# Optimization experiments

Hardware: AMD Instinct MI355X
Metric: run time of the kernel (lower is better)

The kernel has to match this reference:

```python
import jax, jax.numpy as jnp
import numpy as np
from jax.scipy.linalg import solve_triangular

B, T, D = 4, 8192, 1024
HEAD_DIM = 128
CHUNK = 64


def setup_inputs() -> dict:
    key = jax.random.key(0)
    ks = jax.random.split(key, 8)
    H = D // HEAD_DIM
    x = jax.random.normal(ks[0], (B, T, D), dtype=jnp.float32)
    W_write = jax.random.normal(ks[1], (D, D), dtype=jnp.float32) * 0.02
    W_gate = jax.random.normal(ks[2], (H, D), dtype=jnp.float32) * 0.02
    W_out = jax.random.normal(ks[3], (D, D), dtype=jnp.float32) * 0.02
    W_beta = jax.random.normal(ks[4], (H, D), dtype=jnp.float32) * 0.02
    W_alpha = jax.random.normal(ks[5], (H, D), dtype=jnp.float32) * 0.02
    # dt_bias init as in torch: dt ~ loguniform(1e-3, 1e-1), bias = dt + log(-expm1(-dt))
    u = jax.random.uniform(ks[6], (H,), dtype=jnp.float32)
    dt = jnp.exp(u * (jnp.log(jnp.float32(0.1)) - jnp.log(jnp.float32(0.001))) + jnp.log(jnp.float32(0.001)))
    dt_bias = dt + jnp.log(-jnp.expm1(-dt))
    A_log = jnp.log(jax.random.uniform(ks[7], (H,), dtype=jnp.float32, minval=1e-3, maxval=16.0))
    return {"x": x, "W_write": W_write, "W_gate": W_gate, "W_out": W_out,
            "W_beta": W_beta, "W_alpha": W_alpha, "dt_bias": dt_bias, "A_log": A_log}


def reference(x, W_write, W_gate, W_out, W_beta, W_alpha, dt_bias, A_log):
    Bn, Tn, Dm = x.shape
    H = A_log.shape[0]
    d = Dm // H
    C = CHUNK
    assert Tn % C == 0
    N = Tn // C

    xf = x.astype(jnp.float32)
    v = (xf @ W_write.T).reshape(Bn, Tn, H, d)                       # write values
    gate = jax.nn.sigmoid(xf @ W_gate.T)[..., None]                  # (B,T,H,1)
    beta = jax.nn.sigmoid(xf @ W_beta.T)                             # (B,T,H)
    decay = -jnp.exp(A_log) * jax.nn.softplus(xf @ W_alpha.T + dt_bias)  # (B,T,H)

    rk = xf.reshape(Bn, Tn, H, d)
    rk = rk / jnp.maximum(jnp.linalg.norm(rk, axis=-1, keepdims=True), 1e-12)
    wk = jnp.pad(rk[:, :-1], ((0, 0), (1, 0), (0, 0), (0, 0)))       # token-shifted write key

    # (B,H,T,d)
    rk = rk.transpose(0, 2, 1, 3)
    wk = wk.transpose(0, 2, 1, 3)
    v = v.transpose(0, 2, 1, 3)
    bt = beta.transpose(0, 2, 1)[..., None]
    v = v * bt
    wk_beta = wk * bt

    # chunked: (B,H,N,C,d)
    rk = rk.reshape(Bn, H, N, C, d)
    wk = wk.reshape(Bn, H, N, C, d)
    v = v.reshape(Bn, H, N, C, d)
    wk_beta = wk_beta.reshape(Bn, H, N, C, d)
    dec = jnp.cumsum(decay.transpose(0, 2, 1).reshape(Bn, H, N, C), axis=-1)  # cumulative log-decay
    dec_exp = jnp.exp(dec)[..., None]

    lower = jnp.tril(jnp.ones((C, C), dtype=bool))            # incl. diagonal
    strict_lower = jnp.tril(jnp.ones((C, C), dtype=bool), -1)
    diff = dec[..., :, None] - dec[..., None, :]
    L_mask = jnp.exp(jnp.where(lower, diff, -jnp.inf))        # (B,H,N,C,C), 0 above diag

    # UT transform: torch's in-place row loop computes (I + M_strict)^{-1}
    M = jnp.einsum('bhnid,bhnjd->bhnij', wk_beta, wk) * L_mask
    M = jnp.where(strict_lower, M, jnp.float32(0.0))
    eye = jnp.eye(C, dtype=jnp.float32)
    A = solve_triangular(eye + M, jnp.broadcast_to(eye, M.shape), lower=True)

    v = A @ v
    wk_cumdecay = A @ (wk_beta * dec_exp)

    # sequential inter-chunk recurrence over N chunks, carrying matrix state S
    xs = (rk.transpose(2, 0, 1, 3, 4), wk.transpose(2, 0, 1, 3, 4), v.transpose(2, 0, 1, 3, 4),
          wk_cumdecay.transpose(2, 0, 1, 3, 4), dec.transpose(2, 0, 1, 3), L_mask.transpose(2, 0, 1, 3, 4))
    S0 = jnp.zeros((Bn, H, d, d), dtype=jnp.float32)

    def step(S, inp):
        rk_i, wk_i, v_i, wkcd_i, dec_i, L_i = inp
        attn = jnp.einsum('bhid,bhjd->bhij', rk_i, wk_i) * L_i
        attn = jnp.where(lower, attn, jnp.float32(0.0))
        v_new = v_i - wkcd_i @ S
        o_i = (rk_i * jnp.exp(dec_i)[..., None]) @ S + attn @ v_new
        dw = jnp.exp(dec_i[..., -1:] - dec_i)[..., None]                  # (B,H,C,1)
        S_new = S * jnp.exp(dec_i[..., -1])[..., None, None] + jnp.einsum('bhcd,bhce->bhde', wk_i * dw, v_new)
        return S_new, o_i

    _, o = jax.lax.scan(step, S0, xs)                 # (N,B,H,C,d)
    o = o.transpose(1, 2, 0, 3, 4).reshape(Bn, H, Tn, d).transpose(0, 2, 1, 3)  # (B,T,H,d)
    o = (o * gate).reshape(Bn, Tn, Dm)
    return (x + (o @ W_out.T)).astype(x.dtype)
```

## Files before the change

### kernel.cpp

```cpp
#include <hip/hip_runtime.h>
#include <math.h>

#define B_ 4
#define T_ 8192
#define D_ 1024
#define H_ 8
#define HD_ 128
#define C_ 64
#define N_ 128
#define BT_ (B_*T_)
#define BH_ (B_*H_)

typedef unsigned short ushort_t;
typedef unsigned long long ull_t;
typedef short s8v __attribute__((ext_vector_type(8)));
typedef float f32x4 __attribute__((ext_vector_type(4)));

__device__ __forceinline__ void fma4(float4& a, float s, const float4& v) {
  a.x += s*v.x; a.y += s*v.y; a.z += s*v.z; a.w += s*v.w;
}
__device__ __forceinline__ float bfu(unsigned int u16) {
  return __uint_as_float(u16 << 16);
}
__device__ __forceinline__ ushort_t f2bf(float f) {
  unsigned int x = __float_as_uint(f);
  x += 0x7FFFu + ((x >> 16) & 1u);
  return (ushort_t)(x >> 16);
}
__device__ __forceinline__ ull_t pack4bf(float a, float b, float c, float d) {
  return (ull_t)f2bf(a) | ((ull_t)f2bf(b) << 16) | ((ull_t)f2bf(c) << 32) | ((ull_t)f2bf(d) << 48);
}

__global__ __launch_bounds__(256) void k1_proj(
    const float* __restrict__ x, const float* __restrict__ Wg,
    const float* __restrict__ Wb, const float* __restrict__ Wa,
    const float* __restrict__ dt_bias, const float* __restrict__ A_log,
    float* __restrict__ gate_buf, float* __restrict__ beta_buf,
    float* __restrict__ decay_buf, float* __restrict__ innorm_buf) {
  const int row = blockIdx.x;
  const int b = row / T_, t = row % T_;
  const int tid = threadIdx.x;
  __shared__ float xs[D_];
  __shared__ float red[3][H_][4];
  __shared__ float scal[3][H_];
  __shared__ float rnorm[H_];

  ((float4*)xs)[tid] = ((const float4*)(x + (size_t)row * D_))[tid];
  __syncthreads();

  float pg[H_], pb[H_], pa[H_];
  #pragma unroll
  for (int h = 0; h < H_; h++) { pg[h] = 0.f; pb[h] = 0.f; pa[h] = 0.f; }
  for (int i = tid; i < D_; i += 256) {
    float xv = xs[i];
    #pragma unroll
    for (int h = 0; h < H_; h++) {
      pg[h] += xv * Wg[h*D_ + i];
      pb[h] += xv * Wb[h*D_ + i];
      pa[h] += xv * Wa[h*D_ + i];
    }
  }
  const int lane = tid & 63, wv = tid >> 6;
  #pragma unroll
  for (int h = 0; h < H_; h++) {
    float g = pg[h], bb = pb[h], aa = pa[h];
    #pragma unroll
    for (int off = 32; off > 0; off >>= 1) {
      g  += __shfl_down(g, off);
      bb += __shfl_down(bb, off);
      aa += __shfl_down(aa, off);
    }
    if (lane == 0) { red[0][h][wv] = g; red[1][h][wv] = bb; red[2][h][wv] = aa; }
  }
  float pn;
  {
    int hh = tid >> 5, e0 = (tid & 31) * 4;
    const float* xh = xs + hh*HD_ + e0;
    pn = xh[0]*xh[0] + xh[1]*xh[1] + xh[2]*xh[2] + xh[3]*xh[3];
  }
  #pragma unroll
  for (int off = 16; off > 0; off >>= 1) pn += __shfl_down(pn, off, 32);
  __syncthreads();
  if ((tid & 31) == 0) rnorm[tid >> 5] = fmaxf(sqrtf(pn), 1e-12f);
  if (tid < 24) {
    int p = tid >> 3, h = tid & 7;
    scal[p][h] = red[p][h][0] + red[p][h][1] + red[p][h][2] + red[p][h][3];
  }
  __syncthreads();
  if (tid < H_) {
    int h = tid;
    float g  = 1.f / (1.f + expf(-scal[0][h]));
    float be = 1.f / (1.f + expf(-scal[1][h]));
    float z  = scal[2][h] + dt_bias[h];
    float sp = (z > 20.f) ? z : log1pf(expf(z));
    float dc = -expf(A_log[h]) * sp;
    size_t idx = (size_t)(b*H_ + h)*T_ + t;
    gate_buf[idx] = g; beta_buf[idx] = be; decay_buf[idx] = dc;
    innorm_buf[idx] = 1.f / rnorm[h];
  }
}

__global__ __launch_bounds__(256) void k_gemm_bf16(
    const float* __restrict__ A, const float* __restrict__ W,
    const float* __restrict__ R, float* __restrict__ C,
    int M, int N, int K) {
  __shared__ ushort_t La[128*40];
  __shared__ ushort_t Lw[128*40];
  const int tid = threadIdx.x;
  const int w = tid >> 6, lane = tid & 63;
  const int l15 = lane & 15, l4 = lane >> 4;
  const int wr = w >> 1, wc = w & 1;

  const int nwg = gridDim.x;
  const int NB = N >> 7;
  const int bid = blockIdx.x;
  const int swz = (bid & 7) * (nwg >> 3) + (bid >> 3);
  const int row0 = (swz / NB) * 128, col0 = (swz % NB) * 128;

  f32x4 acc[4][4];
  #pragma unroll
  for (int m = 0; m < 4; m++)
    #pragma unroll
    for (int n = 0; n < 4; n++)
      #pragma unroll
      for (int r = 0; r < 4; r++) acc[m][n][r] = 0.f;

  float4 pa[2][2], pw[2][2];
  auto LOAD = [&](int k0) {
    #pragma unroll
    for (int s = 0; s < 2; s++) {
      int slot = tid + s*256;
      int rw = slot >> 2, kg = (slot & 3) * 8;
      const float* ap = A + (size_t)(row0 + rw)*K + k0 + kg;
      pa[s][0] = *(const float4*)ap; pa[s][1] = *(const float4*)(ap + 4);
      const float* wp = W + (size_t)(col0 + rw)*K + k0 + kg;
      pw[s][0] = *(const float4*)wp; pw[s][1] = *(const float4*)(wp + 4);
    }
  };

  LOAD(0);
  for (int k0 = 0; k0 < K; k0 += 32) {
    #pragma unroll
    for (int s = 0; s < 2; s++) {
      int slot = tid + s*256;
      int rw = slot >> 2, kg = (slot & 3) * 8;
      int4 ua, uw;
      ua.x = (int)f2bf(pa[s][0].x) | ((int)f2bf(pa[s][0].y) << 16);
      ua.y = (int)f2bf(pa[s][0].z) | ((int)f2bf(pa[s][0].w) << 16);
      ua.z = (int)f2bf(pa[s][1].x) | ((int)f2bf(pa[s][1].y) << 16);
      ua.w = (int)f2bf(pa[s][1].z) | ((int)f2bf(pa[s][1].w) << 16);
      uw.x = (int)f2bf(pw[s][0].x) | ((int)f2bf(pw[s][0].y) << 16);
      uw.y = (int)f2bf(pw[s][0].z) | ((int)f2bf(pw[s][0].w) << 16);
      uw.z = (int)f2bf(pw[s][1].x) | ((int)f2bf(pw[s][1].y) << 16);
      uw.w = (int)f2bf(pw[s][1].z) | ((int)f2bf(pw[s][1].w) << 16);
      *(int4*)&La[rw*40 + kg] = ua;
      *(int4*)&Lw[rw*40 + kg] = uw;
    }
    __syncthreads();
    if (k0 + 32 < K) LOAD(k0 + 32);
    s8v af[4], bf[4];
    #pragma unroll
    for (int m = 0; m < 4; m++)
      af[m] = *(const s8v*)&La[(wr*64 + m*16 + l15)*40 + l4*8];
    #pragma unroll
    for (int n = 0; n < 4; n++)
      bf[n] = *(const s8v*)&Lw[(wc*64 + n*16 + l15)*40 + l4*8];
    #pragma unroll
    for (int m = 0; m < 4; m++)
      #pragma unroll
      for (int n = 0; n < 4; n++)
        acc[m][n] = __builtin_amdgcn_mfma_f32_16x16x32_bf16(af[m], bf[n], acc[m][n], 0, 0, 0);
    __syncthreads();
  }

  #pragma unroll
  for (int m = 0; m < 4; m++) {
    #pragma unroll
    for (int r = 0; r < 4; r++) {
      int row = row0 + wr*64 + m*16 + l4*4 + r;
      size_t base = (size_t)row * N + col0 + wc*64 + l15;
      #pragma unroll
      for (int n = 0; n < 4; n++) {
        float v = acc[m][n][r];
        if (R) v += R[base + n*16];
        C[base + n*16] = v;
      }
    }
  }
}

__global__ __launch_bounds__(256) void k3_chunk(
    const float* __restrict__ x, float* __restrict__ v_io,
    const float* __restrict__ beta_buf, const float* __restrict__ decay_buf,
    const float* __restrict__ innorm_buf,
    ushort_t* __restrict__ wkcd_buf, ushort_t* __restrict__ attn_buf,
    float* __restrict__ dec_buf) {
  const int blk = blockIdx.x;
  const int bh = blk >> 7, n = blk & 127;
  const int b = bh >> 3, h = bh & 7;
  const int t0 = n * C_;
  const int tid = threadIdx.x;
  __shared__ float Pool[65*132];
  __shared__ float U[C_][66];
  __shared__ float dec[C_], beta_s[C_], edec[C_], inn[65];

  if (tid < 65) {
    int tg = t0 - 1 + tid;
    inn[tid] = (tg >= 0) ? innorm_buf[(size_t)bh*T_ + tg] : 0.f;
  }
  if (tid >= 192) {
    int i = tid - 192;
    size_t g = (size_t)bh*T_ + t0 + i;
    beta_s[i] = beta_buf[g];
    dec[i] = decay_buf[g];
  }
  __syncthreads();
  for (int idx = tid; idx < 65*32; idx += 256) {
    int i = idx >> 5, e4 = (idx & 31) * 4;
    int tg = t0 - 1 + i;
    float4 v = {0.f,0.f,0.f,0.f};
    if (tg >= 0) {
      v = *(const float4*)&x[((size_t)b*T_ + tg)*D_ + h*HD_ + e4];
      float s = inn[i];
      v.x*=s; v.y*=s; v.z*=s; v.w*=s;
    }
    *(float4*)&Pool[i*132 + e4] = v;
  }
  __syncthreads();
  if (tid == 0) { float s = 0.f; for (int i = 0; i < C_; i++) { s += dec[i]; dec[i] = s; } }
  __syncthreads();
  if (tid < C_) {
    edec[tid] = expf(dec[tid]);
    dec_buf[(size_t)bh*T_ + t0 + tid] = dec[tid];
  }
  const int bi = tid >> 4, bj = tid & 15;
  const int i0m = bi*4, j0m = bj*4;
  if (bi >= bj) {
    float m[4][4] = {{0.f}}, am[4][4] = {{0.f}};
    for (int k = 0; k < HD_; k += 4) {
      float4 wb[4];
      #pragma unroll
      for (int c = 0; c < 4; c++) wb[c] = *(const float4*)&Pool[(j0m+c)*132 + k];
      #pragma unroll
      for (int r = 0; r < 4; r++) {
        float4 wa = *(const float4*)&Pool[(i0m+r)*132 + k];
        float4 ra = *(const float4*)&Pool[(i0m+1+r)*132 + k];
        #pragma unroll
        for (int c = 0; c < 4; c++) {
          m[r][c]  += wa.x*wb[c].x + wa.y*wb[c].y + wa.z*wb[c].z + wa.w*wb[c].w;
          am[r][c] += ra.x*wb[c].x + ra.y*wb[c].y + ra.z*wb[c].z + ra.w*wb[c].w;
        }
      }
    }
    #pragma unroll
    for (int r = 0; r < 4; r++) {
      int i = i0m + r;
      #pragma unroll
      for (int c = 0; c < 4; c++) {
        int j = j0m + c;
        if (j < i) U[i][j] = m[r][c] * beta_s[i] * expf(dec[i]-dec[j]);
      }
      float a0 = (j0m+0 <= i) ? am[r][0]*expf(dec[i]-dec[j0m+0]) : 0.f;
      float a1 = (j0m+1 <= i) ? am[r][1]*expf(dec[i]-dec[j0m+1]) : 0.f;
      float a2 = (j0m+2 <= i) ? am[r][2]*expf(dec[i]-dec[j0m+2]) : 0.f;
      float a3 = (j0m+3 <= i) ? am[r][3]*expf(dec[i]-dec[j0m+3]) : 0.f;
      *(ull_t*)&attn_buf[(((size_t)bh*N_ + n)*C_ + i)*C_ + j0m] = pack4bf(a0,a1,a2,a3);
    }
  } else {
    #pragma unroll
    for (int r = 0; r < 4; r++) {
      int i = i0m + r;
      *(ull_t*)&attn_buf[(((size_t)bh*N_ + n)*C_ + i)*C_ + j0m] = 0ull;
    }
  }
  __syncthreads();
  if (tid < C_) {
    int j = tid;
    U[j][j] = 1.f;
    for (int i = j + 1; i < C_; i++) {
      float s = 0.f;
      for (int l = j; l < i; l++) s += U[i][l] * U[j][l];
      U[j][i] = -s;
    }
  }
  __syncthreads();
  for (int idx = tid; idx < C_*32; idx += 256) {
    int i = idx >> 5, e4 = (idx & 31) * 4;
    float s = beta_s[i] * edec[i];
    float4 v = *(const float4*)&Pool[i*132 + e4];
    v.x*=s; v.y*=s; v.z*=s; v.w*=s;
    *(float4*)&Pool[i*132 + e4] = v;
  }
  __syncthreads();
  const int i0 = (tid >> 4) * 4, e0 = (tid & 15) * 8;
  {
    float acc[4][8];
    #pragma unroll
    for (int r = 0; r < 4; r++)
      #pragma unroll
      for (int c = 0; c < 8; c++) acc[r][c] = 0.f;
    for (int j = 0; j < i0; j++) {
      float a0=U[j][i0], a1=U[j][i0+1], a2=U[j][i0+2], a3=U[j][i0+3];
      float4 w0 = *(const float4*)&Pool[j*132 + e0];
      float4 w1 = *(const float4*)&Pool[j*132 + e0 + 4];
      float ww[8] = {w0.x,w0.y,w0.z,w0.w,w1.x,w1.y,w1.z,w1.w};
      float aa[4] = {a0,a1,a2,a3};
      #pragma unroll
      for (int r = 0; r < 4; r++)
        #pragma unroll
        for (int c = 0; c < 8; c++) acc[r][c] += aa[r]*ww[c];
    }
    #pragma unroll
    for (int jj = 0; jj < 4; jj++) {
      int j = i0 + jj;
      float4 w0 = *(const float4*)&Pool[j*132 + e0];
      float4 w1 = *(const float4*)&Pool[j*132 + e0 + 4];
      float ww[8] = {w0.x,w0.y,w0.z,w0.w,w1.x,w1.y,w1.z,w1.w};
      for (int r = jj; r < 4; r++) {
        float a = U[j][i0+r];
        #pragma unroll
        for (int c = 0; c < 8; c++) acc[r][c] += a*ww[c];
      }
    }
    #pragma unroll
    for (int r = 0; r < 4; r++) {
      size_t base = ((size_t)bh*T_ + t0 + i0 + r)*HD_ + e0;
      *(ull_t*)&wkcd_buf[base]   = pack4bf(acc[r][0],acc[r][1],acc[r][2],acc[r][3]);
      *(ull_t*)&wkcd_buf[base+4] = pack4bf(acc[r][4],acc[r][5],acc[r][6],acc[r][7]);
    }
  }
  __syncthreads();
  for (int idx = tid; idx < C_*32; idx += 256) {
    int i = idx >> 5, e4 = (idx & 31) * 4;
    float4 v = *(const float4*)&v_io[((size_t)b*T_ + t0 + i)*D_ + h*HD_ + e4];
    float s = beta_s[i];
    v.x*=s; v.y*=s; v.z*=s; v.w*=s;
    *(float4*)&Pool[i*128 + e4] = v;
  }
  __syncthreads();
  {
    float acc[4][8];
    #pragma unroll
    for (int r = 0; r < 4; r++)
      #pragma unroll
      for (int c = 0; c < 8; c++) acc[r][c] = 0.f;
    for (int j = 0; j < i0; j++) {
      float aa[4] = {U[j][i0], U[j][i0+1], U[j][i0+2], U[j][i0+3]};
      float4 v0 = *(const float4*)&Pool[j*128 + e0];
      float4 v1 = *(const float4*)&Pool[j*128 + e0 + 4];
      float vv[8] = {v0.x,v0.y,v0.z,v0.w,v1.x,v1.y,v1.z,v1.w};
      #pragma unroll
      for (int r = 0; r < 4; r++)
        #pragma unroll
        for (int c = 0; c < 8; c++) acc[r][c] += aa[r]*vv[c];
    }
    #pragma unroll
    for (int jj = 0; jj < 4; jj++) {
      int j = i0 + jj;
      float4 v0 = *(const float4*)&Pool[j*128 + e0];
      float4 v1 = *(const float4*)&Pool[j*128 + e0 + 4];
      float vv[8] = {v0.x,v0.y,v0.z,v0.w,v1.x,v1.y,v1.z,v1.w};
      for (int r = jj; r < 4; r++) {
        float a = U[j][i0+r];
        #pragma unroll
        for (int c = 0; c < 8; c++) acc[r][c] += a*vv[c];
      }
    }
    #pragma unroll
    for (int r = 0; r < 4; r++) {
      size_t base = ((size_t)b*T_ + t0 + i0 + r)*D_ + h*HD_ + e0;
      float4 v0 = {acc[r][0],acc[r][1],acc[r][2],acc[r][3]};
      float4 v1 = {acc[r][4],acc[r][5],acc[r][6],acc[r][7]};
      *(float4*)&v_io[base]     = v0;
      *(float4*)&v_io[base + 4] = v1;
    }
  }
}

__global__ __launch_bounds__(512, 2) void k4_mfma(
    const float* __restrict__ x, float* __restrict__ v_io,
    const ushort_t* __restrict__ wkcd_buf, const ushort_t* __restrict__ attn_buf,
    const float* __restrict__ dec_buf, const float* __restrict__ gate_buf,
    const float* __restrict__ innorm_buf) {
  const int bh = blockIdx.x >> 2;
  const int eq = blockIdx.x & 3;
  const int e0b = eq * 32;
  const int b = bh >> 3, h = bh & 7;
  const int tid = threadIdx.x;
  const int w = tid >> 6, lane = tid & 63;
  const int l15 = lane & 15, l4 = lane >> 4;
  const int mt = w >> 1, nt = w & 1;

  __shared__ ushort_t Krm[64*136];
  __shared__ ushort_t Kt [128*72];
  __shared__ ushort_t Wn [64*136];
  __shared__ ushort_t At [64*72];
  __shared__ ushort_t Sth[32*136];
  __shared__ ushort_t Stl[32*136];
  __shared__ ushort_t Vt [32*72];
  __shared__ float dec_s[64], gate_s[64], sc_s[64], dwn_s[64];

  f32x4 Sacc[2];
  #pragma unroll
  for (int et = 0; et < 2; et++)
    #pragma unroll
    for (int r = 0; r < 4; r++) Sacc[et][r] = 0.f;

  float4 kf[5], wf[2], af;

  auto PF = [&](int nn) {
    const int tb = nn * C_ - 1;
    #pragma unroll
    for (int k = 0; k < 5; k++) {
      int idx = tid + 512*k;
      float4 v = {0.f,0.f,0.f,0.f};
      if (idx < 2080) {
        int row = idx >> 5, q = idx & 31;
        int tg = tb + row;
        if (tg >= 0) v = *(const float4*)&x[((size_t)b*T_ + tg)*D_ + h*HD_ + q*4];
      }
      kf[k] = v;
    }
    #pragma unroll
    for (int k = 0; k < 2; k++) {
      int p = tid + 512*k;
      wf[k] = *(const float4*)&wkcd_buf[((size_t)bh*T_ + nn*C_)*HD_ + p*8];
    }
    af = *(const float4*)&attn_buf[(((size_t)bh*N_ + nn)*C_)*C_ + (size_t)tid*8];
  };

  PF(0);

  for (int n = 0; n < N_; n++) {
    const int t0 = n * C_;
    #pragma unroll
    for (int k = 0; k < 5; k++) {
      int idx = tid + 512*k;
      if (idx < 2080) {
        int row = idx >> 5, q = idx & 31;
        float4 v = kf[k];
        ushort_t b0 = f2bf(v.x), b1 = f2bf(v.y), b2 = f2bf(v.z), b3 = f2bf(v.w);
        if (row >= 1)
          *(ull_t*)&Krm[(row-1)*136 + q*4] =
              (ull_t)b0 | ((ull_t)b1<<16) | ((ull_t)b2<<32) | ((ull_t)b3<<48);
        if (row <= 63) {
          Kt[(q*4+0)*72 + row] = b0;
          Kt[(q*4+1)*72 + row] = b1;
          Kt[(q*4+2)*72 + row] = b2;
          Kt[(q*4+3)*72 + row] = b3;
        }
      }
    }
    #pragma unroll
    for (int k = 0; k < 2; k++) {
      int p = tid + 512*k;
      int row = p >> 4, col = (p & 15) * 8;
      int4 u = *(int4*)&wf[k];
      u.x ^= 0x80008000; u.y ^= 0x80008000; u.z ^= 0x80008000; u.w ^= 0x80008000;
      *(int4*)&Wn[row*136 + col] = u;
    }
    {
      int row = tid >> 3, col = (tid & 7) * 8;
      *(float4*)&At[row*72 + col] = af;
    }
    #pragma unroll
    for (int et = 0; et < 2; et++) {
      int e = et*16 + l15;
      int d0 = w*16 + l4*4;
      ull_t ph = 0, pl = 0;
      #pragma unroll
      for (int r = 0; r < 4; r++) {
        float s = Sacc[et][r];
        ushort_t hb = f2bf(s);
        ushort_t lb = f2bf(s - bfu(hb));
        ph |= (ull_t)hb << (16*r);
        pl |= (ull_t)lb << (16*r);
      }
      *(ull_t*)&Sth[e*136 + d0] = ph;
      *(ull_t*)&Stl[e*136 + d0] = pl;
    }
    float vpf[4];
    #pragma unroll
    for (int r = 0; r < 4; r++)
      vpf[r] = v_io[((size_t)b*T_ + t0 + mt*16 + l4*4 + r)*D_ + h*HD_ + e0b + nt*16 + l15];
    float ipr = 0.f, icr = 0.f;
    if (tid < 64) {
      size_t g = (size_t)bh*T_ + t0 + tid;
      dec_s[tid]  = dec_buf[g];
      gate_s[tid] = gate_buf[g];
      icr = innorm_buf[g];
      ipr = (t0 - 1 + tid >= 0) ? innorm_buf[g - 1] : 0.f;
    }
    __syncthreads();
    if (tid < 64) {
      float dv = dec_s[tid], d63 = dec_s[63];
      sc_s[tid]  = expf(dv) * icr;
      dwn_s[tid] = expf(d63 - dv) * ipr;
    }
    if (n + 1 < N_) PF(n + 1);
    f32x4 acc;
    acc[0] = vpf[0]; acc[1] = vpf[1]; acc[2] = vpf[2]; acc[3] = vpf[3];
    #pragma unroll
    for (int ks = 0; ks < 4; ks++) {
      s8v a  = *(const s8v*)&Wn [(mt*16 + l15)*136 + ks*32 + l4*8];
      s8v sh = *(const s8v*)&Sth[(nt*16 + l15)*136 + ks*32 + l4*8];
      s8v sl = *(const s8v*)&Stl[(nt*16 + l15)*136 + ks*32 + l4*8];
      acc = __builtin_amdgcn_mfma_f32_16x16x32_bf16(a, sh, acc, 0, 0, 0);
      acc = __builtin_amdgcn_mfma_f32_16x16x32_bf16(a, sl, acc, 0, 0, 0);
    }
    {
      ull_t pv = 0;
      #pragma unroll
      for (int r = 0; r < 4; r++) pv |= (ull_t)f2bf(acc[r]) << (16*r);
      *(ull_t*)&Vt[(nt*16 + l15)*72 + mt*16 + l4*4] = pv;
    }
    __syncthreads();
    {
      f32x4 o;
      o[0] = 0.f; o[1] = 0.f; o[2] = 0.f; o[3] = 0.f;
      #pragma unroll
      for (int ks = 0; ks < 4; ks++) {
        s8v a  = *(const s8v*)&Krm[(mt*16 + l15)*136 + ks*32 + l4*8];
        s8v sh = *(const s8v*)&Sth[(nt*16 + l15)*136 + ks*32 + l4*8];
        s8v sl = *(const s8v*)&Stl[(nt*16 + l15)*136 + ks*32 + l4*8];
        o = __builtin_amdgcn_mfma_f32_16x16x32_bf16(a, sh, o, 0, 0, 0);
        o = __builtin_amdgcn_mfma_f32_16x16x32_bf16(a, sl, o, 0, 0, 0);
      }
      #pragma unroll
      for (int r = 0; r < 4; r++) o[r] *= sc_s[mt*16 + l4*4 + r];
      #pragma unroll
      for (int ks = 0; ks < 2; ks++) {
        s8v a  = *(const s8v*)&At[(mt*16 + l15)*72 + ks*32 + l4*8];
        s8v bv = *(const s8v*)&Vt[(nt*16 + l15)*72 + ks*32 + l4*8];
        o = __builtin_amdgcn_mfma_f32_16x16x32_bf16(a, bv, o, 0, 0, 0);
      }
      #pragma unroll
      for (int r = 0; r < 4; r++) {
        float g = gate_s[mt*16 + l4*4 + r];
        v_io[((size_t)b*T_ + t0 + mt*16 + l4*4 + r)*D_ + h*HD_ + e0b + nt*16 + l15] = o[r] * g;
      }
    }
    {
      float el = expf(dec_s[63]);
      #pragma unroll
      for (int et = 0; et < 2; et++)
        #pragma unroll
        for (int r = 0; r < 4; r++) Sacc[et][r] *= el;
      s8v a0, a1;
      #pragma unroll
      for (int ks = 0; ks < 2; ks++) {
        s8v kt = *(const s8v*)&Kt[(w*16 + l15)*72 + ks*32 + l4*8];
        int i0 = ks*32 + l4*8;
        s8v am;
        #pragma unroll
        for (int e = 0; e < 8; e++) {
          float f = bfu((ushort_t)kt[e]) * dwn_s[i0 + e];
          am[e] = (short)f2bf(f);
        }
        if (ks == 0) a0 = am; else a1 = am;
      }
      #pragma unroll
      for (int et = 0; et < 2; et++) {
        s8v b0 = *(const s8v*)&Vt[(et*16 + l15)*72 +      l4*8];
        s8v b1 = *(const s8v*)&Vt[(et*16 + l15)*72 + 32 + l4*8];
        Sacc[et] = __builtin_amdgcn_mfma_f32_16x16x32_bf16(a0, b0, Sacc[et], 0, 0, 0);
        Sacc[et] = __builtin_amdgcn_mfma_f32_16x16x32_bf16(a1, b1, Sacc[et], 0, 0, 0);
      }
    }
    __syncthreads();
  }
}

extern "C" void kernel_launch(void* const* d_in, const int* in_sizes, int n_in,
                              void* d_out, int out_size, void* d_ws, size_t ws_size,
                              hipStream_t stream) {
  const float* x       = (const float*)d_in[0];
  const float* W_write = (const float*)d_in[1];
  const float* W_gate  = (const float*)d_in[2];
  const float* W_out   = (const float*)d_in[3];
  const float* W_beta  = (const float*)d_in[4];
  const float* W_alpha = (const float*)d_in[5];
  const float* dt_bias = (const float*)d_in[6];
  const float* A_log   = (const float*)d_in[7];
  float* out = (float*)d_out;

  const size_t SZ_BIG   = (size_t)BT_ * D_;
  const size_t SZ_ATTN  = (size_t)BH_ * N_ * C_ * C_;
  const size_t SZ_SMALL = (size_t)BH_ * T_;

  float*    vraw = (float*)d_ws;
  ushort_t* wkcd = (ushort_t*)(vraw + SZ_BIG);
  ushort_t* attn = wkcd + SZ_BIG;
  float*    decb = (float*)(attn + SZ_ATTN);
  float*    gateb  = decb + SZ_SMALL;
  float*    betab  = gateb + SZ_SMALL;
  float*    decayb = betab + SZ_SMALL;
  float*    innorm = decayb + SZ_SMALL;

  const int GEMM_GRID = (BT_/128) * (D_/128);

  k1_proj<<<BT_, 256, 0, stream>>>(x, W_gate, W_beta, W_alpha, dt_bias, A_log,
                                   gateb, betab, decayb, innorm);
  k_gemm_bf16<<<GEMM_GRID, 256, 0, stream>>>(x, W_write, nullptr, vraw,
                                             BT_, D_, D_);
  k3_chunk<<<BH_*N_, 256, 0, stream>>>(x, vraw, betab, decayb, innorm,
                                       wkcd, attn, decb);
  k4_mfma<<<BH_*4, 512, 0, stream>>>(x, vraw, wkcd, attn, decb, gateb, innorm);
  k_gemm_bf16<<<GEMM_GRID, 256, 0, stream>>>(vraw, W_out, x, out,
                                             BT_, D_, D_);
}
```

Measured before the change: 1.668 ms.

## Split recurrence kernel over 8 value-column slices with warp specialization and XCD mapping

The sequential chunk recurrence kernel now splits each (batch, head) across 8 blocks of 16 value columns instead of 4 blocks of 32, doubling the grid to 256 blocks. Block IDs are remapped so all slices of one head land on the same XCD. Within a block, warps are specialized: four warps compute the corrected values while the other four concurrently compute the state-times-query output. The transposed key shared buffer is replaced by direct per-lane global loads of the shifted key. The aim is more parallelism and shorter per-step latency on the serial scan, at the cost of reading x and the write-key/attention inputs redundantly across more blocks.

```diff
diff --git a/kernel.cpp b/kernel.cpp
--- a/kernel.cpp
+++ b/kernel.cpp
@@ -382,51 +382,45 @@
     const ushort_t* __restrict__ wkcd_buf, const ushort_t* __restrict__ attn_buf,
     const float* __restrict__ dec_buf, const float* __restrict__ gate_buf,
     const float* __restrict__ innorm_buf) {
-  const int bh = blockIdx.x >> 2;
-  const int eq = blockIdx.x & 3;
-  const int e0b = eq * 32;
+  const int bid = blockIdx.x;
+  const int xcd = bid & 7, jj = bid >> 3;
+  const int bh = xcd*4 + (jj >> 3);
+  const int eq = jj & 7;
+  const int e0b = eq * 16;
   const int b = bh >> 3, h = bh & 7;
   const int tid = threadIdx.x;
   const int w = tid >> 6, lane = tid & 63;
   const int l15 = lane & 15, l4 = lane >> 4;
-  const int mt = w >> 1, nt = w & 1;
+  const bool lowg = (w < 4);
+  const int mw = w & 3;
 
   __shared__ ushort_t Krm[64*136];
-  __shared__ ushort_t Kt [128*72];
   __shared__ ushort_t Wn [64*136];
   __shared__ ushort_t At [64*72];
-  __shared__ ushort_t Sth[32*136];
-  __shared__ ushort_t Stl[32*136];
-  __shared__ ushort_t Vt [32*72];
+  __shared__ ushort_t Sth[16*136];
+  __shared__ ushort_t Stl[16*136];
+  __shared__ ushort_t Vt [16*72];
   __shared__ float dec_s[64], gate_s[64], sc_s[64], dwn_s[64];
 
-  f32x4 Sacc[2];
-  #pragma unroll
-  for (int et = 0; et < 2; et++)
-    #pragma unroll
-    for (int r = 0; r < 4; r++) Sacc[et][r] = 0.f;
-
-  float4 kf[5], wf[2], af;
-
+  f32x4 Sacc;
+  Sacc[0]=0.f; Sacc[1]=0.f; Sacc[2]=0.f; Sacc[3]=0.f;
+
+  float4 kf[4], wf[2], af;
   auto PF = [&](int nn) {
-    const int tb = nn * C_ - 1;
-    #pragma unroll
-    for (int k = 0; k < 5; k++) {
-      int idx = tid + 512*k;
-      float4 v = {0.f,0.f,0.f,0.f};
-      if (idx < 2080) {
-        int row = idx >> 5, q = idx & 31;
-        int tg = tb + row;
-        if (tg >= 0) v = *(const float4*)&x[((size_t)b*T_ + tg)*D_ + h*HD_ + q*4];
-      }
-      kf[k] = v;
+    const int t0n = nn * C_;
+    #pragma unroll
+    for (int k = 0; k < 4; k++) {
+      int slot = tid + 512*k;
+      int row = slot >> 5, q = slot & 31;
+      kf[k] = *(const float4*)&x[((size_t)b*T_ + t0n + row)*D_ + h*HD_ + q*4];
     }
     #pragma unroll
     for (int k = 0; k < 2; k++) {
       int p = tid + 512*k;
-      wf[k] = *(const float4*)&wkcd_buf[((size_t)bh*T_ + nn*C_)*HD_ + p*8];
-    }
-    af = *(const float4*)&attn_buf[(((size_t)bh*N_ + nn)*C_)*C_ + (size_t)tid*8];
+      int row = p >> 4, cg = p & 15;
+      wf[k] = *(const float4*)&wkcd_buf[((size_t)bh*T_ + t0n + row)*HD_ + cg*8];
+    }
+    af = *(const float4*)&attn_buf[(((size_t)bh*N_ + nn)*C_ + (tid>>3))*C_ + (tid&7)*8];
   };
 
   PF(0);
@@ -434,55 +428,49 @@
   for (int n = 0; n < N_; n++) {
     const int t0 = n * C_;
     #pragma unroll
-    for (int k = 0; k < 5; k++) {
-      int idx = tid + 512*k;
-      if (idx < 2080) {
-        int row = idx >> 5, q = idx & 31;
-        float4 v = kf[k];
-        ushort_t b0 = f2bf(v.x), b1 = f2bf(v.y), b2 = f2bf(v.z), b3 = f2bf(v.w);
-        if (row >= 1)
-          *(ull_t*)&Krm[(row-1)*136 + q*4] =
-              (ull_t)b0 | ((ull_t)b1<<16) | ((ull_t)b2<<32) | ((ull_t)b3<<48);
-        if (row <= 63) {
-          Kt[(q*4+0)*72 + row] = b0;
-          Kt[(q*4+1)*72 + row] = b1;
-          Kt[(q*4+2)*72 + row] = b2;
-          Kt[(q*4+3)*72 + row] = b3;
-        }
-      }
+    for (int k = 0; k < 4; k++) {
+      int slot = tid + 512*k;
+      int row = slot >> 5, q = slot & 31;
+      float4 v = kf[k];
+      *(ull_t*)&Krm[row*136 + q*4] = pack4bf(v.x, v.y, v.z, v.w);
     }
     #pragma unroll
     for (int k = 0; k < 2; k++) {
       int p = tid + 512*k;
-      int row = p >> 4, col = (p & 15) * 8;
+      int row = p >> 4, cg = p & 15;
       int4 u = *(int4*)&wf[k];
       u.x ^= 0x80008000; u.y ^= 0x80008000; u.z ^= 0x80008000; u.w ^= 0x80008000;
-      *(int4*)&Wn[row*136 + col] = u;
-    }
+      *(int4*)&Wn[row*136 + cg*8] = u;
+    }
+    *(int4*)&At[(tid>>3)*72 + (tid&7)*8] = *(int4*)&af;
     {
-      int row = tid >> 3, col = (tid & 7) * 8;
-      *(float4*)&At[row*72 + col] = af;
-    }
-    #pragma unroll
-    for (int et = 0; et < 2; et++) {
-      int e = et*16 + l15;
-      int d0 = w*16 + l4*4;
       ull_t ph = 0, pl = 0;
       #pragma unroll
       for (int r = 0; r < 4; r++) {
-        float s = Sacc[et][r];
+        float s = Sacc[r];
         ushort_t hb = f2bf(s);
         ushort_t lb = f2bf(s - bfu(hb));
         ph |= (ull_t)hb << (16*r);
         pl |= (ull_t)lb << (16*r);
       }
-      *(ull_t*)&Sth[e*136 + d0] = ph;
-      *(ull_t*)&Stl[e*136 + d0] = pl;
-    }
-    float vpf[4];
-    #pragma unroll
-    for (int r = 0; r < 4; r++)
-      vpf[r] = v_io[((size_t)b*T_ + t0 + mt*16 + l4*4 + r)*D_ + h*HD_ + e0b + nt*16 + l15];
+      *(ull_t*)&Sth[l15*136 + w*16 + l4*4] = ph;
+      *(ull_t*)&Stl[l15*136 + w*16 + l4*4] = pl;
+    }
+    float vpf[4] = {0.f, 0.f, 0.f, 0.f};
+    if (lowg) {
+      #pragma unroll
+      for (int r = 0; r < 4; r++)
+        vpf[r] = v_io[((size_t)b*T_ + t0 + mw*16 + l4*4 + r)*D_ + h*HD_ + e0b + l15];
+    }
+    float ktf[16];
+    #pragma unroll
+    for (int ks = 0; ks < 2; ks++)
+      #pragma unroll
+      for (int j2 = 0; j2 < 8; j2++) {
+        int tg = t0 - 1 + ks*32 + l4*8 + j2;
+        ktf[ks*8+j2] = (tg >= 0)
+            ? x[((size_t)b*T_ + tg)*D_ + h*HD_ + w*16 + l15] : 0.f;
+      }
     float ipr = 0.f, icr = 0.f;
     if (tid < 64) {
       size_t g = (size_t)bh*T_ + t0 + tid;
@@ -498,73 +486,61 @@
       dwn_s[tid] = expf(d63 - dv) * ipr;
     }
     if (n + 1 < N_) PF(n + 1);
-    f32x4 acc;
-    acc[0] = vpf[0]; acc[1] = vpf[1]; acc[2] = vpf[2]; acc[3] = vpf[3];
-    #pragma unroll
-    for (int ks = 0; ks < 4; ks++) {
-      s8v a  = *(const s8v*)&Wn [(mt*16 + l15)*136 + ks*32 + l4*8];
-      s8v sh = *(const s8v*)&Sth[(nt*16 + l15)*136 + ks*32 + l4*8];
-      s8v sl = *(const s8v*)&Stl[(nt*16 + l15)*136 + ks*32 + l4*8];
-      acc = __builtin_amdgcn_mfma_f32_16x16x32_bf16(a, sh, acc, 0, 0, 0);
-      acc = __builtin_amdgcn_mfma_f32_16x16x32_bf16(a, sl, acc, 0, 0, 0);
-    }
-    {
+    f32x4 oacc;
+    if (lowg) {
+      f32x4 acc;
+      acc[0]=vpf[0]; acc[1]=vpf[1]; acc[2]=vpf[2]; acc[3]=vpf[3];
+      #pragma unroll
+      for (int ks = 0; ks < 4; ks++) {
+        s8v a  = *(const s8v*)&Wn [(mw*16 + l15)*136 + ks*32 + l4*8];
+        s8v sh = *(const s8v*)&Sth[l15*136 + ks*32 + l4*8];
+        s8v sl = *(const s8v*)&Stl[l15*136 + ks*32 + l4*8];
+        acc = __builtin_amdgcn_mfma_f32_16x16x32_bf16(a, sh, acc, 0, 0, 0);
+        acc = __builtin_amdgcn_mfma_f32_16x16x32_bf16(a, sl, acc, 0, 0, 0);
+      }
       ull_t pv = 0;
       #pragma unroll
       for (int r = 0; r < 4; r++) pv |= (ull_t)f2bf(acc[r]) << (16*r);
-      *(ull_t*)&Vt[(nt*16 + l15)*72 + mt*16 + l4*4] = pv;
+      *(ull_t*)&Vt[l15*72 + mw*16 + l4*4] = pv;
+    } else {
+      oacc[0]=0.f; oacc[1]=0.f; oacc[2]=0.f; oacc[3]=0.f;
+      #pragma unroll
+      for (int ks = 0; ks < 4; ks++) {
+        s8v a  = *(const s8v*)&Krm[(mw*16 + l15)*136 + ks*32 + l4*8];
+        s8v sh = *(const s8v*)&Sth[l15*136 + ks*32 + l4*8];
+        s8v sl = *(const s8v*)&Stl[l15*136 + ks*32 + l4*8];
+        oacc = __builtin_amdgcn_mfma_f32_16x16x32_bf16(a, sh, oacc, 0, 0, 0);
+        oacc = __builtin_amdgcn_mfma_f32_16x16x32_bf16(a, sl, oacc, 0, 0, 0);
+      }
     }
     __syncthreads();
-    {
-      f32x4 o;
-      o[0] = 0.f; o[1] = 0.f; o[2] = 0.f; o[3] = 0.f;
-      #pragma unroll
-      for (int ks = 0; ks < 4; ks++) {
-        s8v a  = *(const s8v*)&Krm[(mt*16 + l15)*136 + ks*32 + l4*8];
-        s8v sh = *(const s8v*)&Sth[(nt*16 + l15)*136 + ks*32 + l4*8];
-        s8v sl = *(const s8v*)&Stl[(nt*16 + l15)*136 + ks*32 + l4*8];
-        o = __builtin_amdgcn_mfma_f32_16x16x32_bf16(a, sh, o, 0, 0, 0);
-        o = __builtin_amdgcn_mfma_f32_16x16x32_bf16(a, sl, o, 0, 0, 0);
-      }
-      #pragma unroll
-      for (int r = 0; r < 4; r++) o[r] *= sc_s[mt*16 + l4*4 + r];
+    if (!lowg) {
+      #pragma unroll
+      for (int r = 0; r < 4; r++) oacc[r] *= sc_s[mw*16 + l4*4 + r];
       #pragma unroll
       for (int ks = 0; ks < 2; ks++) {
-        s8v a  = *(const s8v*)&At[(mt*16 + l15)*72 + ks*32 + l4*8];
-        s8v bv = *(const s8v*)&Vt[(nt*16 + l15)*72 + ks*32 + l4*8];
-        o = __builtin_amdgcn_mfma_f32_16x16x32_bf16(a, bv, o, 0, 0, 0);
+        s8v a  = *(const s8v*)&At[(mw*16 + l15)*72 + ks*32 + l4*8];
+        s8v bv = *(const s8v*)&Vt[l15*72 + ks*32 + l4*8];
+        oacc = __builtin_amdgcn_mfma_f32_16x16x32_bf16(a, bv, oacc, 0, 0, 0);
       }
       #pragma unroll
       for (int r = 0; r < 4; r++) {
-        float g = gate_s[mt*16 + l4*4 + r];
-        v_io[((size_t)b*T_ + t0 + mt*16 + l4*4 + r)*D_ + h*HD_ + e0b + nt*16 + l15] = o[r] * g;
+        float g = gate_s[mw*16 + l4*4 + r];
+        v_io[((size_t)b*T_ + t0 + mw*16 + l4*4 + r)*D_ + h*HD_ + e0b + l15] = oacc[r] * g;
       }
     }
     {
       float el = expf(dec_s[63]);
       #pragma unroll
-      for (int et = 0; et < 2; et++)
-        #pragma unroll
-        for (int r = 0; r < 4; r++) Sacc[et][r] *= el;
-      s8v a0, a1;
+      for (int r = 0; r < 4; r++) Sacc[r] *= el;
       #pragma unroll
       for (int ks = 0; ks < 2; ks++) {
-        s8v kt = *(const s8v*)&Kt[(w*16 + l15)*72 + ks*32 + l4*8];
-        int i0 = ks*32 + l4*8;
         s8v am;
         #pragma unroll
-        for (int e = 0; e < 8; e++) {
-          float f = bfu((ushort_t)kt[e]) * dwn_s[i0 + e];
-          am[e] = (short)f2bf(f);
-        }
-        if (ks == 0) a0 = am; else a1 = am;
-      }
-      #pragma unroll
-      for (int et = 0; et < 2; et++) {
-        s8v b0 = *(const s8v*)&Vt[(et*16 + l15)*72 +      l4*8];
-        s8v b1 = *(const s8v*)&Vt[(et*16 + l15)*72 + 32 + l4*8];
-        Sacc[et] = __builtin_amdgcn_mfma_f32_16x16x32_bf16(a0, b0, Sacc[et], 0, 0, 0);
-        Sacc[et] = __builtin_amdgcn_mfma_f32_16x16x32_bf16(a1, b1, Sacc[et], 0, 0, 0);
+        for (int j2 = 0; j2 < 8; j2++)
+          am[j2] = (short)f2bf(ktf[ks*8+j2] * dwn_s[ks*32 + l4*8 + j2]);
+        s8v bv = *(const s8v*)&Vt[l15*72 + ks*32 + l4*8];
+        Sacc = __builtin_amdgcn_mfma_f32_16x16x32_bf16(am, bv, Sacc, 0, 0, 0);
       }
     }
     __syncthreads();
@@ -605,7 +581,7 @@
                                              BT_, D_, D_);
   k3_chunk<<<BH_*N_, 256, 0, stream>>>(x, vraw, betab, decayb, innorm,
                                        wkcd, attn, decb);
-  k4_mfma<<<BH_*4, 512, 0, stream>>>(x, vraw, wkcd, attn, decb, gateb, innorm);
+  k4_mfma<<<BH_*8, 512, 0, stream>>>(x, vraw, wkcd, attn, decb, gateb, innorm);
   k_gemm_bf16<<<GEMM_GRID, 256, 0, stream>>>(vraw, W_out, x, out,
                                              BT_, D_, D_);
 }
```

Measured after the change: 1.487 ms. 10.9% less time.
